# Performance work log

Hardware: AMD Instinct MI355X
Metric: run time of the kernel (lower is better)

## Reference

```python
import jax, jax.numpy as jnp
import numpy as np

B, N, NC, D, DC, L, NH = 8, 512, 256, 512, 256, 12, 8
DK = D // NH


def _ln(x, g, b, eps=1e-5):
    m = x.mean(-1, keepdims=True)
    v = ((x - m) ** 2).mean(-1, keepdims=True)
    return (x - m) * jax.lax.rsqrt(v + eps) * g + b


def setup_inputs() -> dict:
    key = jax.random.key(0)
    ks = iter(jax.random.split(key, 64))
    def rn(shape, s=1.0):
        return jax.random.normal(next(ks), shape, dtype=jnp.float32) * s
    w = 0.02
    inp = {
        "x_t": rn((B, N, 2)),
        "a_t": jax.random.uniform(next(ks), (B, N, N), dtype=jnp.float32),
        "hdse_node": rn((B, N, D), 0.1),
        "hdse_bias": rn((B, NH, N, N), 0.1),
        "context": rn((B, NC, DC)),
        "coord_w": rn((2, D), w), "coord_b": jnp.zeros((D,)),
        "deg_w": rn((1, D), w), "deg_b": jnp.zeros((D,)),
        "tm_w1": rn((D, 4 * D), w), "tm_b1": jnp.zeros((4 * D,)),
        "tm_w2": rn((4 * D, D), w), "tm_b2": jnp.zeros((D,)),
        "ln_sa_g": jnp.ones((L, D)), "ln_sa_b": jnp.zeros((L, D)),
        "qkv_w": rn((L, D, 3 * D), w), "qkv_b": jnp.zeros((L, 3 * D)),
        "osa_w": rn((L, D, D), w), "osa_b": jnp.zeros((L, D)),
        "ln_ca_g": jnp.ones((L, D)), "ln_ca_b": jnp.zeros((L, D)),
        "qca_w": rn((L, D, D), w), "qca_b": jnp.zeros((L, D)),
        "kvca_w": rn((L, DC, 2 * D), w), "kvca_b": jnp.zeros((L, 2 * D)),
        "oca_w": rn((L, D, D), w), "oca_b": jnp.zeros((L, D)),
        "ln_ff_g": jnp.ones((L, D)), "ln_ff_b": jnp.zeros((L, D)),
        "ff1_w": rn((L, D, 4 * D), w), "ff1_b": jnp.zeros((L, 4 * D)),
        "ff2_w": rn((L, 4 * D, D), w), "ff2_b": jnp.zeros((L, D)),
        "fn_g": jnp.ones((D,)), "fn_b": jnp.zeros((D,)),
        "ch_w": rn((D, 2), w), "ch_b": jnp.zeros((2,)),
        "es_w": rn((D, D // 4), w), "es_b": jnp.zeros((D // 4,)),
        "ed_w": rn((D, D // 4), w), "ed_b": jnp.zeros((D // 4,)),
        "eb": jnp.zeros((1,)),
        "t": jax.random.randint(next(ks), (B,), 0, 1000),
        "node_mask": jnp.ones((B, N), dtype=bool),
        "context_mask": jnp.ones((B, NC), dtype=bool),
    }
    return inp


def reference(x_t, a_t, hdse_node, hdse_bias, context,
              coord_w, coord_b, deg_w, deg_b,
              tm_w1, tm_b1, tm_w2, tm_b2,
              ln_sa_g, ln_sa_b, qkv_w, qkv_b, osa_w, osa_b,
              ln_ca_g, ln_ca_b, qca_w, qca_b, kvca_w, kvca_b, oca_w, oca_b,
              ln_ff_g, ln_ff_b, ff1_w, ff1_b, ff2_w, ff2_b,
              fn_g, fn_b, ch_w, ch_b, es_w, es_b, ed_w, ed_b, eb,
              t, node_mask, context_mask):
    scale = 1.0 / np.sqrt(DK).astype(np.float32)
    # input embedding: coords + degree + timestep + HDSE node encodings
    h = x_t @ coord_w + coord_b
    h = h + a_t.sum(-1, keepdims=True) @ deg_w + deg_b
    half = D // 2
    freqs = jnp.exp(-jnp.log(10000.0) * jnp.arange(half, dtype=jnp.float32) / half)
    ang = t.astype(jnp.float32)[:, None] * freqs[None, :]
    emb = jnp.concatenate([jnp.sin(ang), jnp.cos(ang)], -1)
    temb = jax.nn.gelu(emb @ tm_w1 + tm_b1, approximate=False) @ tm_w2 + tm_b2
    h = h + temb[:, None, :] + hdse_node
    nmask = node_mask[:, None, None, :]
    cmask = context_mask[:, None, None, :]
    for i in range(L):
        # self-attention with HDSE bias
        hn = _ln(h, ln_sa_g[i], ln_sa_b[i])
        qkv = (hn @ qkv_w[i] + qkv_b[i]).reshape(B, N, 3, NH, DK)
        q, k, v = [jnp.moveaxis(qkv[:, :, j], 1, 2) for j in range(3)]  # (B,NH,N,DK)
        s = jnp.einsum('bhnd,bhmd->bhnm', q, k) * scale + hdse_bias
        s = jnp.where(nmask, s, -1e9)
        sa = jnp.einsum('bhnm,bhmd->bhnd', jax.nn.softmax(s, -1), v)
        sa = jnp.moveaxis(sa, 1, 2).reshape(B, N, D)
        h = h + sa @ osa_w[i] + osa_b[i]
        # cross-attention to context
        hn = _ln(h, ln_ca_g[i], ln_ca_b[i])
        q = jnp.moveaxis((hn @ qca_w[i] + qca_b[i]).reshape(B, N, NH, DK), 1, 2)
        kv = (context @ kvca_w[i] + kvca_b[i]).reshape(B, NC, 2, NH, DK)
        kc = jnp.moveaxis(kv[:, :, 0], 1, 2)
        vc = jnp.moveaxis(kv[:, :, 1], 1, 2)
        s = jnp.einsum('bhnd,bhmd->bhnm', q, kc) * scale
        s = jnp.where(cmask, s, -1e9)
        ca = jnp.einsum('bhnm,bhmd->bhnd', jax.nn.softmax(s, -1), vc)
        ca = jnp.moveaxis(ca, 1, 2).reshape(B, N, D)
        h = h + ca @ oca_w[i] + oca_b[i]
        # FFN
        hn = _ln(h, ln_ff_g[i], ln_ff_b[i])
        h = h + jax.nn.gelu(hn @ ff1_w[i] + ff1_b[i], approximate=False) @ ff2_w[i] + ff2_b[i]
    h = _ln(h, fn_g, fn_b)
    eps = h @ ch_w + ch_b
    hs = h @ es_w + es_b
    hd = h @ ed_w + ed_b
    el = jnp.einsum('bne,bme->bnm', hs, hd) + eb[0]
    el = (el + jnp.swapaxes(el, 1, 2)) * 0.5
    el = jnp.where(jnp.eye(N, dtype=bool)[None], 0.0, el)
    eps = eps * node_mask[..., None].astype(eps.dtype)
    pm = node_mask[:, :, None] & node_mask[:, None, :]
    el = jnp.where(pm, el, 0.0)
    return eps, el
```

## Files before the change

### kernel.cpp

```cpp
#include <hip/hip_runtime.h>


#define DEV static __device__ __forceinline__

typedef __attribute__((ext_vector_type(8))) short short8;
typedef __attribute__((ext_vector_type(4))) short short4v;
typedef __attribute__((ext_vector_type(4))) float f32x4;

DEV float b2f(unsigned short u) {
    union { unsigned int i; float f; } x; x.i = ((unsigned int)u) << 16; return x.f;
}
DEV unsigned short f2b(float f) {
    union { float f; unsigned int i; } x; x.f = f;
    unsigned int i = x.i;
    return (unsigned short)((i + 0x7fffu + ((i >> 16) & 1u)) >> 16);
}
DEV float gelu_exact(float x) { return 0.5f * x * (1.0f + erff(x * 0.70710678118654752440f)); }

DEV void load_lds16(const unsigned short* g, unsigned short* l) {
    __builtin_amdgcn_global_load_lds(
        (const __attribute__((address_space(1))) unsigned int*)g,
        (__attribute__((address_space(3))) unsigned int*)l, 16, 0, 0);
}

#define S_VMCNT(n) asm volatile("s_waitcnt vmcnt(" #n ")" ::: "memory")
#define S_LGKMCNT0 asm volatile("s_waitcnt lgkmcnt(0)" ::: "memory")

template<int BM, int BN, int EPI>
__launch_bounds__(256)
__global__ void gemm_bt(const unsigned short* __restrict__ A, int lda, long sA1, long sA2,
                        const unsigned short* __restrict__ Bt, int ldb, long sB1, long sB2,
                        void* __restrict__ Cv, int ldc, long sC1, long sC2,
                        const float* __restrict__ bias,
                        int K, int NZ2)
{
    constexpr int WM = BM / 2, WN = BN / 2;
    constexpr int MF = WM / 16, NF = WN / 16;
    constexpr int LA = BM / 64, LB = BN / 64;
    constexpr int L = LA + LB;
    __shared__ __align__(16) unsigned short lA0[BM * 32];
    __shared__ __align__(16) unsigned short lA1[BM * 32];
    __shared__ __align__(16) unsigned short lB0[BN * 32];
    __shared__ __align__(16) unsigned short lB1[BN * 32];

    const int tid = threadIdx.x;
    const int lane = tid & 63, wave = tid >> 6;
    const int quad = lane >> 4, l16 = lane & 15;
    const int wm = wave >> 1, wn = wave & 1;

    const int z = blockIdx.z;
    const int z1 = z / NZ2, z2 = z - z1 * NZ2;
    const unsigned short* Ab = A + z1 * sA1 + z2 * sA2 + (long)blockIdx.y * BM * lda;
    const unsigned short* Bb = Bt + z1 * sB1 + z2 * sB2 + (long)blockIdx.x * BN * ldb;

    const int srow = tid >> 2, scol = (tid & 3) * 8;

    f32x4 acc[MF][NF] = {};

    auto stage = [&](unsigned short* dA, unsigned short* dB, int k0) {
        #pragma unroll
        for (int i = 0; i < LA; i++)
            load_lds16(Ab + (long)(srow + i * 64) * lda + k0 + scol,
                       dA + (srow + i * 64) * 32 + scol);
        #pragma unroll
        for (int i = 0; i < LB; i++)
            load_lds16(Bb + (long)(srow + i * 64) * ldb + k0 + scol,
                       dB + (srow + i * 64) * 32 + scol);
    };

    const int nk = K >> 5;
    stage(lA0, lB0, 0);
    stage(lA1, lB1, 32);

    auto step = [&](int t, unsigned short* cA, unsigned short* cB) {
        if (t + 1 < nk) { if constexpr (L == 3) S_VMCNT(3); else S_VMCNT(4); }
        else            S_VMCNT(0);
        __builtin_amdgcn_s_barrier();
        __builtin_amdgcn_sched_barrier(0);
        short8 af[MF], bf[NF];
        #pragma unroll
        for (int m = 0; m < MF; m++)
            af[m] = *(const short8*)&cA[(wm * WM + m * 16 + l16) * 32 + quad * 8];
        #pragma unroll
        for (int n = 0; n < NF; n++)
            bf[n] = *(const short8*)&cB[(wn * WN + n * 16 + l16) * 32 + quad * 8];
        S_LGKMCNT0;
        __builtin_amdgcn_s_barrier();
        __builtin_amdgcn_sched_barrier(0);
        if (t + 2 < nk) stage(cA, cB, (t + 2) << 5);
        #pragma unroll
        for (int m = 0; m < MF; m++)
            #pragma unroll
            for (int n = 0; n < NF; n++)
                acc[m][n] = __builtin_amdgcn_mfma_f32_16x16x32_bf16(af[m], bf[n], acc[m][n], 0, 0, 0);
    };

    for (int t = 0; t < nk; t += 2) {
        step(t,     lA0, lB0);
        step(t + 1, lA1, lB1);
    }

    const long cb = z1 * sC1 + z2 * sC2;
    const int r0 = blockIdx.y * BM + wm * WM + quad * 4;
    const int c0 = blockIdx.x * BN + wn * WN + l16;
    #pragma unroll
    for (int m = 0; m < MF; m++) {
        #pragma unroll
        for (int n = 0; n < NF; n++) {
            const int c = c0 + n * 16;
            float bvv = 0.f;
            if (EPI == 0 || EPI == 1 || EPI == 2) bvv = bias ? bias[c] : 0.f;
            #pragma unroll
            for (int t2 = 0; t2 < 4; t2++) {
                const int r = r0 + m * 16 + t2;
                const float v = acc[m][n][t2];
                const long idx = cb + (long)r * ldc + c;
                if (EPI == 0) {
                    ((unsigned short*)Cv)[idx] = f2b(v + bvv);
                } else if (EPI == 1) {
                    ((unsigned short*)Cv)[idx] = f2b(gelu_exact(v + bvv));
                } else if (EPI == 2) {
                    float* Cf = (float*)Cv;
                    Cf[idx] = Cf[idx] + v + bvv;
                } else {
                    ((float*)Cv)[idx] = v;
                }
            }
        }
    }
}

template<int NKT, bool HB>
__launch_bounds__(256)
__global__ void attn_fused(const unsigned short* __restrict__ Qp, int ldq,
                           const unsigned short* __restrict__ Kp, int ldk,
                           const unsigned short* __restrict__ Vt,
                           const unsigned short* __restrict__ biasp,
                           unsigned short* __restrict__ Out)
{
    constexpr int KEYS = NKT * 128;
    __shared__ __align__(16) unsigned short kbuf[8192];
    __shared__ __align__(16) unsigned short vbuf[8192];
    __shared__ __align__(16) unsigned short pbuf[8192];

    const int tid = threadIdx.x;
    const int lane = tid & 63, w = tid >> 6;
    const int quad = lane >> 4, l16 = lane & 15;
    const int qblk = blockIdx.x;
    const int bh = blockIdx.y;
    const int b = bh >> 3, hh = bh & 7;

    const unsigned short* Q = Qp + (long)(b * 512 + qblk * 64) * ldq + hh * 64;
    const unsigned short* K = Kp + (long)b * KEYS * ldk + hh * 64;
    const unsigned short* V = Vt + (long)bh * 64 * KEYS;
    const unsigned short* Bi = HB ? biasp + (long)bh * 262144 + (long)(qblk * 64) * 512 : nullptr;
    unsigned short* O = Out + (long)(b * 512 + qblk * 64) * 512 + hh * 64;

    const short8 a0 = *(const short8*)(Q + (long)(w * 16 + l16) * ldq + quad * 8);
    const short8 a1 = *(const short8*)(Q + (long)(w * 16 + l16) * ldq + 32 + quad * 8);

    f32x4 acc[NKT * 8];
    #pragma unroll
    for (int f = 0; f < NKT * 8; f++) acc[f] = f32x4{0.f, 0.f, 0.f, 0.f};

    for (int kt = 0; kt < NKT; kt++) {
        __syncthreads();
        #pragma unroll
        for (int p = 0; p < 4; p++) {
            const int key = p * 32 + (tid >> 3);
            const int col = (tid & 7) * 8;
            short8 v = *(const short8*)(K + (long)(kt * 128 + key) * ldk + col);
            *(short8*)&kbuf[(col >> 5) * 4096 + key * 32 + (col & 31)] = v;
        }
        __syncthreads();
        #pragma unroll
        for (int nf = 0; nf < 8; nf++) {
            const short8 b0 = *(const short8*)&kbuf[(nf * 16 + l16) * 32 + quad * 8];
            const short8 b1 = *(const short8*)&kbuf[4096 + (nf * 16 + l16) * 32 + quad * 8];
            acc[kt * 8 + nf] = __builtin_amdgcn_mfma_f32_16x16x32_bf16(a0, b0, acc[kt * 8 + nf], 0, 0, 0);
            acc[kt * 8 + nf] = __builtin_amdgcn_mfma_f32_16x16x32_bf16(a1, b1, acc[kt * 8 + nf], 0, 0, 0);
        }
    }

    float rmax[4] = {-1e30f, -1e30f, -1e30f, -1e30f};
    #pragma unroll
    for (int f = 0; f < NKT * 8; f++) {
        const int col = (f >> 3) * 128 + (f & 7) * 16 + l16;
        #pragma unroll
        for (int j = 0; j < 4; j++) {
            float v = acc[f][j] * 0.125f;
            if (HB) v += b2f(Bi[(long)(w * 16 + quad * 4 + j) * 512 + col]);
            acc[f][j] = v;
            rmax[j] = fmaxf(rmax[j], v);
        }
    }
    #pragma unroll
    for (int m = 1; m < 16; m <<= 1)
        #pragma unroll
        for (int j = 0; j < 4; j++) rmax[j] = fmaxf(rmax[j], __shfl_xor(rmax[j], m, 64));
    float rsum[4] = {0.f, 0.f, 0.f, 0.f};
    #pragma unroll
    for (int f = 0; f < NKT * 8; f++)
        #pragma unroll
        for (int j = 0; j < 4; j++) {
            const float e = __expf(acc[f][j] - rmax[j]);
            acc[f][j] = e;
            rsum[j] += e;
        }
    #pragma unroll
    for (int m = 1; m < 16; m <<= 1)
        #pragma unroll
        for (int j = 0; j < 4; j++) rsum[j] += __shfl_xor(rsum[j], m, 64);
    float rinv[4];
    #pragma unroll
    for (int j = 0; j < 4; j++) rinv[j] = 1.f / rsum[j];

    f32x4 oacc[4];
    #pragma unroll
    for (int c = 0; c < 4; c++) oacc[c] = f32x4{0.f, 0.f, 0.f, 0.f};

    for (int kt = 0; kt < NKT; kt++) {
        __syncthreads();
        #pragma unroll
        for (int p = 0; p < 4; p++) {
            const int dk = p * 16 + (tid >> 4);
            const int keyloc = (tid & 15) * 8;
            short8 v = *(const short8*)(V + (long)dk * KEYS + kt * 128 + keyloc);
            *(short8*)&vbuf[(keyloc >> 5) * 2048 + dk * 32 + (keyloc & 31)] = v;
        }
        #pragma unroll
        for (int nf = 0; nf < 8; nf++) {
            const int keyloc = nf * 16 + l16;
            #pragma unroll
            for (int j = 0; j < 4; j++)
                pbuf[(keyloc >> 5) * 2048 + (w * 16 + quad * 4 + j) * 32 + (keyloc & 31)]
                    = f2b(acc[kt * 8 + nf][j] * rinv[j]);
        }
        __syncthreads();
        #pragma unroll
        for (int ks = 0; ks < 4; ks++) {
            const short8 ap = *(const short8*)&pbuf[ks * 2048 + (w * 16 + l16) * 32 + quad * 8];
            #pragma unroll
            for (int c = 0; c < 4; c++) {
                const short8 bp = *(const short8*)&vbuf[ks * 2048 + (c * 16 + l16) * 32 + quad * 8];
                oacc[c] = __builtin_amdgcn_mfma_f32_16x16x32_bf16(ap, bp, oacc[c], 0, 0, 0);
            }
        }
    }

    #pragma unroll
    for (int c = 0; c < 4; c++)
        #pragma unroll
        for (int j = 0; j < 4; j++)
            O[(long)(w * 16 + quad * 4 + j) * 512 + c * 16 + l16] = f2b(oacc[c][j]);
}

__launch_bounds__(256)
__global__ void ln_kernel(const float* __restrict__ x, const float* __restrict__ g,
                          const float* __restrict__ bb, unsigned short* __restrict__ out)
{
    const int lane = threadIdx.x & 63;
    const long row = (long)blockIdx.x * 4 + (threadIdx.x >> 6);
    const float* xr = x + row * 512 + lane * 8;
    float v[8];
    *(f32x4*)v = *(const f32x4*)xr;
    *(f32x4*)(v + 4) = *(const f32x4*)(xr + 4);
    float s = 0.f;
    #pragma unroll
    for (int j = 0; j < 8; j++) s += v[j];
    #pragma unroll
    for (int m = 1; m < 64; m <<= 1) s += __shfl_xor(s, m, 64);
    const float mean = s * (1.f / 512.f);
    float q = 0.f;
    #pragma unroll
    for (int j = 0; j < 8; j++) { float d = v[j] - mean; q += d * d; }
    #pragma unroll
    for (int m = 1; m < 64; m <<= 1) q += __shfl_xor(q, m, 64);
    const float rstd = rsqrtf(q * (1.f / 512.f) + 1e-5f);
    const int d0 = lane * 8;
    unsigned short o[8];
    #pragma unroll
    for (int j = 0; j < 8; j++) o[j] = f2b((v[j] - mean) * rstd * g[d0 + j] + bb[d0 + j]);
    *(short8*)(out + row * 512 + d0) = *(short8*)o;
}

__launch_bounds__(256)
__global__ void lnf_kernel(const float* __restrict__ x, const float* __restrict__ g,
                           const float* __restrict__ bb, float* __restrict__ out)
{
    const int lane = threadIdx.x & 63;
    const long row = (long)blockIdx.x * 4 + (threadIdx.x >> 6);
    const float* xr = x + row * 512 + lane * 8;
    float v[8];
    *(f32x4*)v = *(const f32x4*)xr;
    *(f32x4*)(v + 4) = *(const f32x4*)(xr + 4);
    float s = 0.f;
    #pragma unroll
    for (int j = 0; j < 8; j++) s += v[j];
    #pragma unroll
    for (int m = 1; m < 64; m <<= 1) s += __shfl_xor(s, m, 64);
    const float mean = s * (1.f / 512.f);
    float q = 0.f;
    #pragma unroll
    for (int j = 0; j < 8; j++) { float d = v[j] - mean; q += d * d; }
    #pragma unroll
    for (int m = 1; m < 64; m <<= 1) q += __shfl_xor(q, m, 64);
    const float rstd = rsqrtf(q * (1.f / 512.f) + 1e-5f);
    const int d0 = lane * 8;
    float o[8];
    #pragma unroll
    for (int j = 0; j < 8; j++) o[j] = (v[j] - mean) * rstd * g[d0 + j] + bb[d0 + j];
    *(f32x4*)(out + row * 512 + d0) = *(const f32x4*)o;
    *(f32x4*)(out + row * 512 + d0 + 4) = *(const f32x4*)(o + 4);
}

__global__ void wtrans(const float* __restrict__ W, unsigned short* __restrict__ WT, int K, int Nc)
{
    __shared__ float tile[32][33];
    const long zoff = (long)blockIdx.z * K * Nc;
    const int c0 = blockIdx.x * 32, k0 = blockIdx.y * 32;
    const int tx = threadIdx.x, ty = threadIdx.y;
    const float* Wz = W + zoff;
    unsigned short* WTz = WT + zoff;
    #pragma unroll
    for (int i = 0; i < 4; i++)
        tile[ty + i * 8][tx] = Wz[(long)(k0 + ty + i * 8) * Nc + c0 + tx];
    __syncthreads();
    #pragma unroll
    for (int i = 0; i < 4; i++)
        WTz[(long)(c0 + ty + i * 8) * K + k0 + tx] = f2b(tile[tx][ty + i * 8]);
}

__global__ void transp(const unsigned short* __restrict__ src, unsigned short* __restrict__ dst,
                       int ldin, int R, long sS1, long sS2, int NZ2, long sDz)
{
    __shared__ unsigned short tile[32][33];
    const int z = blockIdx.z;
    const unsigned short* s = src + (long)(z / NZ2) * sS1 + (long)(z % NZ2) * sS2;
    unsigned short* d = dst + (long)z * sDz;
    const int r0 = blockIdx.x * 32, c0 = blockIdx.y * 32;
    const int tx = threadIdx.x, ty = threadIdx.y;
    #pragma unroll
    for (int i = 0; i < 4; i++)
        tile[ty + i * 8][tx] = s[(long)(r0 + ty + i * 8) * ldin + c0 + tx];
    __syncthreads();
    #pragma unroll
    for (int i = 0; i < 4; i++)
        d[(long)(c0 + ty + i * 8) * R + r0 + tx] = tile[tx][ty + i * 8];
}

__launch_bounds__(256)
__global__ void cast_kernel(const float* __restrict__ in, unsigned short* __restrict__ out, long n4)
{
    const long i = (long)blockIdx.x * 256 + threadIdx.x;
    if (i >= n4) return;
    const f32x4 v = *(const f32x4*)(in + i * 4);
    unsigned short o[4] = { f2b(v.x), f2b(v.y), f2b(v.z), f2b(v.w) };
    *(short4v*)(out + i * 4) = *(short4v*)o;
}

__launch_bounds__(256)
__global__ void rowsum_kernel(const float* __restrict__ a, float* __restrict__ out)
{
    const int lane = threadIdx.x & 63;
    const long row = (long)blockIdx.x * 4 + (threadIdx.x >> 6);
    const float* ar = a + row * 512 + lane * 8;
    const f32x4 v0 = *(const f32x4*)ar, v1 = *(const f32x4*)(ar + 4);
    float s = v0.x + v0.y + v0.z + v0.w + v1.x + v1.y + v1.z + v1.w;
    #pragma unroll
    for (int m = 1; m < 64; m <<= 1) s += __shfl_xor(s, m, 64);
    if (lane == 0) out[row] = s;
}

__launch_bounds__(256)
__global__ void temb1_kernel(const int* __restrict__ t, const unsigned short* __restrict__ w1t,
                             const float* __restrict__ b1, unsigned short* __restrict__ hid)
{
    __shared__ float emb[512];
    const int b = blockIdx.x >> 3, cb = blockIdx.x & 7, tid = threadIdx.x;
    {
        const float fr = expf(-9.21034037197618f * (float)tid * (1.f / 256.f));
        const float ang = (float)t[b] * fr;
        emb[tid] = sinf(ang);
        emb[tid + 256] = cosf(ang);
    }
    __syncthreads();
    const int o = cb * 256 + tid;
    const unsigned short* wr = w1t + (long)o * 512;
    float acc = b1[o];
    for (int k = 0; k < 512; k += 8) {
        unsigned short u[8];
        *(short8*)u = *(const short8*)(wr + k);
        #pragma unroll
        for (int j = 0; j < 8; j++) acc += emb[k + j] * b2f(u[j]);
    }
    hid[b * 2048 + o] = f2b(gelu_exact(acc));
}

__launch_bounds__(256)
__global__ void temb2_kernel(const unsigned short* __restrict__ hid, const unsigned short* __restrict__ w2t,
                             const float* __restrict__ b2, float* __restrict__ temb)
{
    const int b = blockIdx.x >> 1;
    const int o = (blockIdx.x & 1) * 256 + threadIdx.x;
    const unsigned short* hr = hid + b * 2048;
    const unsigned short* wr = w2t + (long)o * 2048;
    float acc = b2[o];
    for (int k = 0; k < 2048; k += 8) {
        unsigned short hu[8], wu[8];
        *(short8*)hu = *(const short8*)(hr + k);
        *(short8*)wu = *(const short8*)(wr + k);
        #pragma unroll
        for (int j = 0; j < 8; j++) acc += b2f(hu[j]) * b2f(wu[j]);
    }
    temb[b * 512 + o] = acc;
}

__launch_bounds__(256)
__global__ void embed_kernel(const float* __restrict__ x_t, const float* __restrict__ deg,
                             const float* __restrict__ coord_w, const float* __restrict__ coord_b,
                             const float* __restrict__ deg_w, const float* __restrict__ deg_b,
                             const float* __restrict__ temb, const float* __restrict__ hdse_node,
                             float* __restrict__ h)
{
    const long i = (long)blockIdx.x * 256 + threadIdx.x;
    const int d = (int)(i & 511);
    const long row = i >> 9;
    const int b = (int)(row >> 9);
    h[i] = x_t[row * 2] * coord_w[d] + x_t[row * 2 + 1] * coord_w[512 + d] + coord_b[d]
         + deg[row] * deg_w[d] + deg_b[d] + temb[b * 512 + d] + hdse_node[i];
}

__launch_bounds__(256)
__global__ void epsf_kernel(const float* __restrict__ hnf, const float* __restrict__ ch_w,
                            const float* __restrict__ ch_b, float* __restrict__ out)
{
    const int lane = threadIdx.x & 63;
    const long row = (long)blockIdx.x * 4 + (threadIdx.x >> 6);
    const float* hr = hnf + row * 512 + lane * 8;
    float v[8];
    *(f32x4*)v = *(const f32x4*)hr;
    *(f32x4*)(v + 4) = *(const f32x4*)(hr + 4);
    float e0 = 0.f, e1 = 0.f;
    const int d0 = lane * 8;
    #pragma unroll
    for (int j = 0; j < 8; j++) {
        e0 += v[j] * ch_w[(d0 + j) * 2];
        e1 += v[j] * ch_w[(d0 + j) * 2 + 1];
    }
    #pragma unroll
    for (int m = 1; m < 64; m <<= 1) { e0 += __shfl_xor(e0, m, 64); e1 += __shfl_xor(e1, m, 64); }
    if (lane == 0) { out[row * 2] = e0 + ch_b[0]; out[row * 2 + 1] = e1 + ch_b[1]; }
}

__launch_bounds__(256)
__global__ void headw2_kernel(const float* __restrict__ hnf,
                              const float* __restrict__ We, const float* __restrict__ be,
                              const float* __restrict__ Wd, const float* __restrict__ bd,
                              float* __restrict__ oe, float* __restrict__ od)
{
    __shared__ __align__(16) float rows[4][512];
    const long r0 = (long)blockIdx.x * 4;
    const int tid = threadIdx.x;
    #pragma unroll
    for (int i = 0; i < 2; i++) {
        const int idx = tid + i * 256;
        *(f32x4*)&rows[idx >> 7][(idx & 127) * 4] = *(const f32x4*)(hnf + r0 * 512 + (long)idx * 4);
    }
    __syncthreads();
    const int row = tid >> 6;
    const int lane = tid & 63;
    const int kh = lane >> 5;
    const int cg = (lane & 31) * 4;
    const float* rw = &rows[row][kh * 256];
    const float* pe = We + (long)(kh * 256) * 128 + cg;
    const float* pd = Wd + (long)(kh * 256) * 128 + cg;
    f32x4 ae = {0.f, 0.f, 0.f, 0.f}, ad = {0.f, 0.f, 0.f, 0.f};
    #pragma unroll 4
    for (int k = 0; k < 256; k++) {
        const float a = rw[k];
        const f32x4 we = *(const f32x4*)(pe + (long)k * 128);
        const f32x4 wd = *(const f32x4*)(pd + (long)k * 128);
        ae.x += a * we.x; ae.y += a * we.y; ae.z += a * we.z; ae.w += a * we.w;
        ad.x += a * wd.x; ad.y += a * wd.y; ad.z += a * wd.z; ad.w += a * wd.w;
    }
    #pragma unroll
    for (int c = 0; c < 4; c++) {
        ae[c] += __shfl_xor(ae[c], 32, 64);
        ad[c] += __shfl_xor(ad[c], 32, 64);
    }
    if (kh == 0) {
        const f32x4 bve = *(const f32x4*)(be + cg);
        const f32x4 bvd = *(const f32x4*)(bd + cg);
        const f32x4 re = {ae.x + bve.x, ae.y + bve.y, ae.z + bve.z, ae.w + bve.w};
        const f32x4 rd = {ad.x + bvd.x, ad.y + bvd.y, ad.z + bvd.z, ad.w + bvd.w};
        *(f32x4*)(oe + (r0 + row) * 128 + cg) = re;
        *(f32x4*)(od + (r0 + row) * 128 + cg) = rd;
    }
}

__launch_bounds__(256)
__global__ void el_kernel(const float* __restrict__ hs, const float* __restrict__ hd,
                          float* __restrict__ el)
{
    __shared__ float sA[32 * 129];
    __shared__ __align__(16) float sB[128 * 36];
    const int b = blockIdx.z;
    const int n0 = blockIdx.y * 32, m0 = blockIdx.x * 32;
    const float* hsb = hs + ((long)b * 512 + n0) * 128;
    const float* hdb = hd + ((long)b * 512 + m0) * 128;
    const int tid = threadIdx.x;
    const int lr = tid >> 3, lc = (tid & 7) * 16;
    #pragma unroll
    for (int j = 0; j < 4; j++) {
        const f32x4 av = *(const f32x4*)(hsb + (long)lr * 128 + lc + j * 4);
        const f32x4 bv = *(const f32x4*)(hdb + (long)lr * 128 + lc + j * 4);
        #pragma unroll
        for (int u = 0; u < 4; u++) {
            sA[lr * 129 + lc + j * 4 + u] = av[u];
            sB[(lc + j * 4 + u) * 36 + lr] = bv[u];
        }
    }
    __syncthreads();
    const int n = tid >> 3, m = (tid & 7) * 4;
    float a0 = 0.f, a1 = 0.f, a2 = 0.f, a3 = 0.f;
    #pragma unroll 4
    for (int k = 0; k < 128; k++) {
        const float a = sA[n * 129 + k];
        const f32x4 bv = *(const f32x4*)&sB[k * 36 + m];
        a0 += a * bv.x; a1 += a * bv.y; a2 += a * bv.z; a3 += a * bv.w;
    }
    float* o = el + ((long)b * 512 + n0 + n) * 512 + m0 + m;
    const f32x4 r = {a0, a1, a2, a3};
    *(f32x4*)o = r;
}

__launch_bounds__(256)
__global__ void sym_kernel(const float* __restrict__ elb, const float* __restrict__ eb,
                           float* __restrict__ out)
{
    const long i = (long)blockIdx.x * 256 + threadIdx.x;
    const int m = (int)(i & 511);
    const long t = i >> 9;
    const int n = (int)(t & 511);
    const int b = (int)(t >> 9);
    const long base = (long)b * 262144;
    out[i] = (n == m) ? 0.f
           : 0.5f * (elb[base + (long)n * 512 + m] + elb[base + (long)m * 512 + n]) + eb[0];
}

extern "C" void kernel_launch(void* const* d_in, const int* in_sizes, int n_in,
                              void* d_out, int out_size, void* d_ws, size_t ws_size,
                              hipStream_t stream)
{
    const float* x_t       = (const float*)d_in[0];
    const float* a_t       = (const float*)d_in[1];
    const float* hdse_node = (const float*)d_in[2];
    const float* hdse_bias = (const float*)d_in[3];
    const float* context   = (const float*)d_in[4];
    const float* coord_w   = (const float*)d_in[5];
    const float* coord_b   = (const float*)d_in[6];
    const float* deg_w     = (const float*)d_in[7];
    const float* deg_b     = (const float*)d_in[8];
    const float* tm_w1     = (const float*)d_in[9];
    const float* tm_b1     = (const float*)d_in[10];
    const float* tm_w2     = (const float*)d_in[11];
    const float* tm_b2     = (const float*)d_in[12];
    const float* ln_sa_g   = (const float*)d_in[13];
    const float* ln_sa_b   = (const float*)d_in[14];
    const float* qkv_w     = (const float*)d_in[15];
    const float* qkv_b     = (const float*)d_in[16];
    const float* osa_w     = (const float*)d_in[17];
    const float* osa_b     = (const float*)d_in[18];
    const float* ln_ca_g   = (const float*)d_in[19];
    const float* ln_ca_b   = (const float*)d_in[20];
    const float* qca_w     = (const float*)d_in[21];
    const float* qca_b     = (const float*)d_in[22];
    const float* kvca_w    = (const float*)d_in[23];
    const float* kvca_b    = (const float*)d_in[24];
    const float* oca_w     = (const float*)d_in[25];
    const float* oca_b     = (const float*)d_in[26];
    const float* ln_ff_g   = (const float*)d_in[27];
    const float* ln_ff_b   = (const float*)d_in[28];
    const float* ff1_w     = (const float*)d_in[29];
    const float* ff1_b     = (const float*)d_in[30];
    const float* ff2_w     = (const float*)d_in[31];
    const float* ff2_b     = (const float*)d_in[32];
    const float* fn_g      = (const float*)d_in[33];
    const float* fn_b      = (const float*)d_in[34];
    const float* ch_w      = (const float*)d_in[35];
    const float* ch_b      = (const float*)d_in[36];
    const float* es_w      = (const float*)d_in[37];
    const float* es_b      = (const float*)d_in[38];
    const float* ed_w      = (const float*)d_in[39];
    const float* ed_b      = (const float*)d_in[40];
    const float* eb        = (const float*)d_in[41];
    const int*   tt        = (const int*)d_in[42];

    char* w = (char*)d_ws;
    size_t off = 0;
    auto alloc = [&](size_t bytes) -> void* {
        void* p = w + off;
        off = (off + bytes + 255) & ~(size_t)255;
        return p;
    };

    unsigned short* qkv_wt  = (unsigned short*)alloc(12UL * 1536 * 512 * 2);
    unsigned short* osa_wt  = (unsigned short*)alloc(12UL * 512 * 512 * 2);
    unsigned short* qca_wt  = (unsigned short*)alloc(12UL * 512 * 512 * 2);
    unsigned short* kvca_wt = (unsigned short*)alloc(12UL * 1024 * 256 * 2);
    unsigned short* oca_wt  = (unsigned short*)alloc(12UL * 512 * 512 * 2);
    unsigned short* ff1_wt  = (unsigned short*)alloc(12UL * 2048 * 512 * 2);
    unsigned short* ff2_wt  = (unsigned short*)alloc(12UL * 512 * 2048 * 2);
    unsigned short* tm1t    = (unsigned short*)alloc(2048UL * 512 * 2);
    unsigned short* tm2t    = (unsigned short*)alloc(512UL * 2048 * 2);
    unsigned short* biasb   = (unsigned short*)alloc(16777216UL * 2);
    unsigned short* ctxb    = (unsigned short*)alloc(524288UL * 2);
    float*          h     = (float*)alloc(4096UL * 512 * 4);
    unsigned short* hn    = (unsigned short*)alloc(4096UL * 512 * 2);
    float*          hnf   = (float*)alloc(4096UL * 512 * 4);
    unsigned short* qkvb  = (unsigned short*)alloc(4096UL * 1536 * 2);
    unsigned short* vt    = (unsigned short*)alloc(64UL * 64 * 512 * 2);
    unsigned short* vtc   = (unsigned short*)alloc(64UL * 64 * 256 * 2);
    unsigned short* attn  = (unsigned short*)alloc(4096UL * 512 * 2);
    unsigned short* qcab  = (unsigned short*)alloc(4096UL * 512 * 2);
    unsigned short* kvb   = (unsigned short*)alloc(2048UL * 1024 * 2);
    unsigned short* ffb   = (unsigned short*)alloc(4096UL * 2048 * 2);
    float*          hsf   = (float*)alloc(4096UL * 128 * 4);
    float*          hdf   = (float*)alloc(4096UL * 128 * 4);
    float*          elbuf = (float*)alloc(8UL * 512 * 512 * 4);
    float*          degb  = (float*)alloc(4096UL * 4);
    unsigned short* thid  = (unsigned short*)alloc(8UL * 2048 * 2);
    float*          tembb = (float*)alloc(8UL * 512 * 4);

    if (off > ws_size) return;

    const dim3 tb(32, 8);

    wtrans<<<dim3(48, 16, 12), tb, 0, stream>>>(qkv_w,  qkv_wt,  512, 1536);
    wtrans<<<dim3(16, 16, 12), tb, 0, stream>>>(osa_w,  osa_wt,  512, 512);
    wtrans<<<dim3(16, 16, 12), tb, 0, stream>>>(qca_w,  qca_wt,  512, 512);
    wtrans<<<dim3(32,  8, 12), tb, 0, stream>>>(kvca_w, kvca_wt, 256, 1024);
    wtrans<<<dim3(16, 16, 12), tb, 0, stream>>>(oca_w,  oca_wt,  512, 512);
    wtrans<<<dim3(64, 16, 12), tb, 0, stream>>>(ff1_w,  ff1_wt,  512, 2048);
    wtrans<<<dim3(16, 64, 12), tb, 0, stream>>>(ff2_w,  ff2_wt,  2048, 512);
    wtrans<<<dim3(64, 16, 1),  tb, 0, stream>>>(tm_w1,  tm1t,    512, 2048);
    wtrans<<<dim3(16, 64, 1),  tb, 0, stream>>>(tm_w2,  tm2t,    2048, 512);
    cast_kernel<<<16384, 256, 0, stream>>>(hdse_bias, biasb, 4194304L);
    cast_kernel<<<512, 256, 0, stream>>>(context, ctxb, 131072L);

    rowsum_kernel<<<1024, 256, 0, stream>>>(a_t, degb);
    temb1_kernel<<<64, 256, 0, stream>>>(tt, tm1t, tm_b1, thid);
    temb2_kernel<<<16, 256, 0, stream>>>(thid, tm2t, tm_b2, tembb);
    embed_kernel<<<8192, 256, 0, stream>>>(x_t, degb, coord_w, coord_b, deg_w, deg_b,
                                           tembb, hdse_node, h);

    for (int l = 0; l < 12; l++) {
        const unsigned short* qkvW  = qkv_wt  + (size_t)l * 1536 * 512;
        const unsigned short* osaW  = osa_wt  + (size_t)l * 512 * 512;
        const unsigned short* qcaW  = qca_wt  + (size_t)l * 512 * 512;
        const unsigned short* kvcaW = kvca_wt + (size_t)l * 1024 * 256;
        const unsigned short* ocaW  = oca_wt  + (size_t)l * 512 * 512;
        const unsigned short* ff1W  = ff1_wt  + (size_t)l * 2048 * 512;
        const unsigned short* ff2W  = ff2_wt  + (size_t)l * 512 * 2048;

        ln_kernel<<<1024, 256, 0, stream>>>(h, ln_sa_g + l * 512, ln_sa_b + l * 512, hn);
        gemm_bt<128, 128, 0><<<dim3(12, 32, 1), 256, 0, stream>>>(
            hn, 512, 0, 0, qkvW, 512, 0, 0, qkvb, 1536, 0, 0,
            qkv_b + l * 1536, 512, 1);
        transp<<<dim3(16, 2, 64), tb, 0, stream>>>(qkvb + 1024, vt, 1536, 512,
                                                   786432L, 64L, 8, 32768L);
        attn_fused<4, true><<<dim3(8, 64), 256, 0, stream>>>(
            qkvb, 1536, qkvb + 512, 1536, vt, biasb, attn);
        gemm_bt<64, 128, 2><<<dim3(4, 64, 1), 256, 0, stream>>>(
            attn, 512, 0, 0, osaW, 512, 0, 0, h, 512, 0, 0,
            osa_b + l * 512, 512, 1);

        ln_kernel<<<1024, 256, 0, stream>>>(h, ln_ca_g + l * 512, ln_ca_b + l * 512, hn);
        gemm_bt<64, 128, 0><<<dim3(4, 64, 1), 256, 0, stream>>>(
            hn, 512, 0, 0, qcaW, 512, 0, 0, qcab, 512, 0, 0,
            qca_b + l * 512, 512, 1);
        gemm_bt<64, 128, 0><<<dim3(8, 32, 1), 256, 0, stream>>>(
            ctxb, 256, 0, 0, kvcaW, 256, 0, 0, kvb, 1024, 0, 0,
            kvca_b + l * 1024, 256, 1);
        transp<<<dim3(8, 2, 64), tb, 0, stream>>>(kvb + 512, vtc, 1024, 256,
                                                  262144L, 64L, 8, 16384L);
        attn_fused<2, false><<<dim3(8, 64), 256, 0, stream>>>(
            qcab, 512, kvb, 1024, vtc, nullptr, attn);
        gemm_bt<64, 128, 2><<<dim3(4, 64, 1), 256, 0, stream>>>(
            attn, 512, 0, 0, ocaW, 512, 0, 0, h, 512, 0, 0,
            oca_b + l * 512, 512, 1);

        ln_kernel<<<1024, 256, 0, stream>>>(h, ln_ff_g + l * 512, ln_ff_b + l * 512, hn);
        gemm_bt<128, 128, 1><<<dim3(16, 32, 1), 256, 0, stream>>>(
            hn, 512, 0, 0, ff1W, 512, 0, 0, ffb, 2048, 0, 0,
            ff1_b + l * 2048, 512, 1);
        gemm_bt<64, 128, 2><<<dim3(4, 64, 1), 256, 0, stream>>>(
            ffb, 2048, 0, 0, ff2W, 2048, 0, 0, h, 512, 0, 0,
            ff2_b + l * 512, 2048, 1);
    }

    lnf_kernel<<<1024, 256, 0, stream>>>(h, fn_g, fn_b, hnf);
    epsf_kernel<<<1024, 256, 0, stream>>>(hnf, ch_w, ch_b, (float*)d_out);
    headw2_kernel<<<1024, 256, 0, stream>>>(hnf, es_w, es_b, ed_w, ed_b, hsf, hdf);
    el_kernel<<<dim3(16, 16, 8), 256, 0, stream>>>(hsf, hdf, elbuf);
    sym_kernel<<<8192, 256, 0, stream>>>(elbuf, eb, (float*)d_out + 8192);
}
```

Before: 2.778 ms.

## Split-K the residual-add GEMMs with atomics and tile the edge-head projection

```diff
diff --git a/kernel.cpp b/kernel.cpp
--- a/kernel.cpp
+++ b/kernel.cpp
@@ -26,7 +26,7 @@
 #define S_VMCNT(n) asm volatile("s_waitcnt vmcnt(" #n ")" ::: "memory")
 #define S_LGKMCNT0 asm volatile("s_waitcnt lgkmcnt(0)" ::: "memory")
 
-template<int BM, int BN, int EPI>
+template<int BM, int BN, int EPI, int SK = 1>
 __launch_bounds__(256)
 __global__ void gemm_bt(const unsigned short* __restrict__ A, int lda, long sA1, long sA2,
                         const unsigned short* __restrict__ Bt, int ldb, long sB1, long sB2,
@@ -49,9 +49,12 @@
     const int wm = wave >> 1, wn = wave & 1;
 
     const int z = blockIdx.z;
-    const int z1 = z / NZ2, z2 = z - z1 * NZ2;
-    const unsigned short* Ab = A + z1 * sA1 + z2 * sA2 + (long)blockIdx.y * BM * lda;
-    const unsigned short* Bb = Bt + z1 * sB1 + z2 * sB2 + (long)blockIdx.x * BN * ldb;
+    const int zk = (SK > 1) ? (z % SK) : 0;
+    const int zb = (SK > 1) ? (z / SK) : z;
+    const int z1 = zb / NZ2, z2 = zb - z1 * NZ2;
+    const int Keff = K / SK;
+    const unsigned short* Ab = A + z1 * sA1 + z2 * sA2 + (long)blockIdx.y * BM * lda + zk * Keff;
+    const unsigned short* Bb = Bt + z1 * sB1 + z2 * sB2 + (long)blockIdx.x * BN * ldb + zk * Keff;
 
     const int srow = tid >> 2, scol = (tid & 3) * 8;
 
@@ -68,7 +71,7 @@
                        dB + (srow + i * 64) * 32 + scol);
     };
 
-    const int nk = K >> 5;
+    const int nk = Keff >> 5;
     stage(lA0, lB0, 0);
     stage(lA1, lB1, 32);
 
@@ -110,6 +113,7 @@
             const int c = c0 + n * 16;
             float bvv = 0.f;
             if (EPI == 0 || EPI == 1 || EPI == 2) bvv = bias ? bias[c] : 0.f;
+            if (SK > 1 && zk != 0) bvv = 0.f;
             #pragma unroll
             for (int t2 = 0; t2 < 4; t2++) {
                 const int r = r0 + m * 16 + t2;
@@ -121,7 +125,8 @@
                     ((unsigned short*)Cv)[idx] = f2b(gelu_exact(v + bvv));
                 } else if (EPI == 2) {
                     float* Cf = (float*)Cv;
-                    Cf[idx] = Cf[idx] + v + bvv;
+                    if (SK > 1) atomicAdd(&Cf[idx], v + bvv);
+                    else        Cf[idx] = Cf[idx] + v + bvv;
                 } else {
                     ((float*)Cv)[idx] = v;
                 }
@@ -454,49 +459,74 @@
 }
 
 __launch_bounds__(256)
-__global__ void headw2_kernel(const float* __restrict__ hnf,
+__global__ void headw3_kernel(const float* __restrict__ hnf,
                               const float* __restrict__ We, const float* __restrict__ be,
                               const float* __restrict__ Wd, const float* __restrict__ bd,
                               float* __restrict__ oe, float* __restrict__ od)
 {
-    __shared__ __align__(16) float rows[4][512];
-    const long r0 = (long)blockIdx.x * 4;
+    __shared__ __align__(16) float sA[2][32 * 36];
+    __shared__ __align__(16) float sW[2][32 * 68];
     const int tid = threadIdx.x;
-    #pragma unroll
-    for (int i = 0; i < 2; i++) {
-        const int idx = tid + i * 256;
-        *(f32x4*)&rows[idx >> 7][(idx & 127) * 4] = *(const f32x4*)(hnf + r0 * 512 + (long)idx * 4);
-    }
-    __syncthreads();
-    const int row = tid >> 6;
-    const int lane = tid & 63;
-    const int kh = lane >> 5;
-    const int cg = (lane & 31) * 4;
-    const float* rw = &rows[row][kh * 256];
-    const float* pe = We + (long)(kh * 256) * 128 + cg;
-    const float* pd = Wd + (long)(kh * 256) * 128 + cg;
-    f32x4 ae = {0.f, 0.f, 0.f, 0.f}, ad = {0.f, 0.f, 0.f, 0.f};
-    #pragma unroll 4
-    for (int k = 0; k < 256; k++) {
-        const float a = rw[k];
-        const f32x4 we = *(const f32x4*)(pe + (long)k * 128);
-        const f32x4 wd = *(const f32x4*)(pd + (long)k * 128);
-        ae.x += a * we.x; ae.y += a * we.y; ae.z += a * we.z; ae.w += a * we.w;
-        ad.x += a * wd.x; ad.y += a * wd.y; ad.z += a * wd.z; ad.w += a * wd.w;
-    }
-    #pragma unroll
-    for (int c = 0; c < 4; c++) {
-        ae[c] += __shfl_xor(ae[c], 32, 64);
-        ad[c] += __shfl_xor(ad[c], 32, 64);
-    }
-    if (kh == 0) {
-        const f32x4 bve = *(const f32x4*)(be + cg);
-        const f32x4 bvd = *(const f32x4*)(bd + cg);
-        const f32x4 re = {ae.x + bve.x, ae.y + bve.y, ae.z + bve.z, ae.w + bve.w};
-        const f32x4 rd = {ad.x + bvd.x, ad.y + bvd.y, ad.z + bvd.z, ad.w + bvd.w};
-        *(f32x4*)(oe + (r0 + row) * 128 + cg) = re;
-        *(f32x4*)(od + (r0 + row) * 128 + cg) = rd;
-    }
+    const int r0 = blockIdx.x * 32;
+    const int bx = blockIdx.y;
+    const float* W   = (bx < 2) ? We : Wd;
+    const float* bb  = (bx < 2) ? be : bd;
+    float*       out = (bx < 2) ? oe : od;
+    const int coff = (bx & 1) * 64;
+
+    const int ar = tid >> 3, ac = (tid & 7) * 4;
+    const int wk = tid >> 3, wc = (tid & 7) * 8;
+    const float* gA = hnf + (long)(r0 + ar) * 512 + ac;
+    const float* gW = W + (long)wk * 128 + coff + wc;
+
+    const int rr = (tid >> 4) * 2;
+    const int cg = (tid & 15) * 4;
+    f32x4 acc0 = {0.f, 0.f, 0.f, 0.f}, acc1 = {0.f, 0.f, 0.f, 0.f};
+
+    auto LOADT = [&](int t, f32x4& a, f32x4& w0, f32x4& w1) {
+        a  = *(const f32x4*)(gA + t * 32);
+        w0 = *(const f32x4*)(gW + (long)t * 32 * 128);
+        w1 = *(const f32x4*)(gW + (long)t * 32 * 128 + 4);
+    };
+    auto WRITET = [&](int buf, const f32x4& a, const f32x4& w0, const f32x4& w1) {
+        *(f32x4*)&sA[buf][ar * 36 + ac] = a;
+        *(f32x4*)&sW[buf][wk * 68 + wc] = w0;
+        *(f32x4*)&sW[buf][wk * 68 + wc + 4] = w1;
+    };
+    auto COMP = [&](int buf) {
+        #pragma unroll
+        for (int k4 = 0; k4 < 8; k4++) {
+            const f32x4 av0 = *(const f32x4*)&sA[buf][rr * 36 + k4 * 4];
+            const f32x4 av1 = *(const f32x4*)&sA[buf][(rr + 1) * 36 + k4 * 4];
+            #pragma unroll
+            for (int j = 0; j < 4; j++) {
+                const f32x4 wv = *(const f32x4*)&sW[buf][(k4 * 4 + j) * 68 + cg];
+                acc0.x += av0[j] * wv.x; acc0.y += av0[j] * wv.y;
+                acc0.z += av0[j] * wv.z; acc0.w += av0[j] * wv.w;
+                acc1.x += av1[j] * wv.x; acc1.y += av1[j] * wv.y;
+                acc1.z += av1[j] * wv.z; acc1.w += av1[j] * wv.w;
+            }
+        }
+    };
+
+    f32x4 a0, w00, w01, a1, w10, w11;
+    LOADT(0, a0, w00, w01);
+    WRITET(0, a0, w00, w01);
+    for (int t = 0; t < 16; t += 2) {
+        LOADT(t + 1, a1, w10, w11);
+        __syncthreads();
+        COMP(0);
+        WRITET(1, a1, w10, w11);
+        if (t + 2 < 16) LOADT(t + 2, a0, w00, w01);
+        __syncthreads();
+        COMP(1);
+        if (t + 2 < 16) WRITET(0, a0, w00, w01);
+    }
+    const f32x4 bv = *(const f32x4*)(bb + coff + cg);
+    const f32x4 o0 = {acc0.x + bv.x, acc0.y + bv.y, acc0.z + bv.z, acc0.w + bv.w};
+    const f32x4 o1 = {acc1.x + bv.x, acc1.y + bv.y, acc1.z + bv.z, acc1.w + bv.w};
+    *(f32x4*)(out + (long)(r0 + rr) * 128 + coff + cg) = o0;
+    *(f32x4*)(out + (long)(r0 + rr + 1) * 128 + coff + cg) = o1;
 }
 
 __launch_bounds__(256)
@@ -672,7 +702,7 @@
                                                    786432L, 64L, 8, 32768L);
         attn_fused<4, true><<<dim3(8, 64), 256, 0, stream>>>(
             qkvb, 1536, qkvb + 512, 1536, vt, biasb, attn);
-        gemm_bt<64, 128, 2><<<dim3(4, 64, 1), 256, 0, stream>>>(
+        gemm_bt<64, 128, 2, 2><<<dim3(4, 64, 2), 256, 0, stream>>>(
             attn, 512, 0, 0, osaW, 512, 0, 0, h, 512, 0, 0,
             osa_b + l * 512, 512, 1);
 
@@ -687,7 +717,7 @@
                                                   262144L, 64L, 8, 16384L);
         attn_fused<2, false><<<dim3(8, 64), 256, 0, stream>>>(
             qcab, 512, kvb, 1024, vtc, nullptr, attn);
-        gemm_bt<64, 128, 2><<<dim3(4, 64, 1), 256, 0, stream>>>(
+        gemm_bt<64, 128, 2, 2><<<dim3(4, 64, 2), 256, 0, stream>>>(
             attn, 512, 0, 0, ocaW, 512, 0, 0, h, 512, 0, 0,
             oca_b + l * 512, 512, 1);
 
@@ -695,14 +725,14 @@
         gemm_bt<128, 128, 1><<<dim3(16, 32, 1), 256, 0, stream>>>(
             hn, 512, 0, 0, ff1W, 512, 0, 0, ffb, 2048, 0, 0,
             ff1_b + l * 2048, 512, 1);
-        gemm_bt<64, 128, 2><<<dim3(4, 64, 1), 256, 0, stream>>>(
+        gemm_bt<64, 128, 2, 2><<<dim3(4, 64, 2), 256, 0, stream>>>(
             ffb, 2048, 0, 0, ff2W, 2048, 0, 0, h, 512, 0, 0,
             ff2_b + l * 512, 2048, 1);
     }
 
     lnf_kernel<<<1024, 256, 0, stream>>>(h, fn_g, fn_b, hnf);
     epsf_kernel<<<1024, 256, 0, stream>>>(hnf, ch_w, ch_b, (float*)d_out);
-    headw2_kernel<<<1024, 256, 0, stream>>>(hnf, es_w, es_b, ed_w, ed_b, hsf, hdf);
+    headw3_kernel<<<dim3(128, 4), 256, 0, stream>>>(hnf, es_w, es_b, ed_w, ed_b, hsf, hdf);
     el_kernel<<<dim3(16, 16, 8), 256, 0, stream>>>(hsf, hdf, elbuf);
     sym_kernel<<<8192, 256, 0, stream>>>(elbuf, eb, (float*)d_out + 8192);
 }
```

After: 2.710 ms. -2.5%, faster.
